# Kernel optimization log

Measured on AMD Instinct MI355X. Metric: run time of the kernel, lower is better.

The kernel has to match this reference:

```python
import jax, jax.numpy as jnp
import numpy as np

N = 100000      # num nodes
E = 1600000     # num edges (avg degree 16)
F_IN = 64       # n_input
F_H = 64        # n_hidden
K = 8           # Chebyshev order
LN_EPS = 1e-5


def setup_inputs() -> dict:
    key = jax.random.key(0)
    k1, k2, k3 = jax.random.split(key, 3)
    x = jax.random.normal(k1, (N, F_IN), dtype=jnp.float32)
    edge_index = jax.random.randint(k2, (2, E), 0, N, dtype=jnp.int32)
    # ChebConv learned params: K weight matrices + bias
    weight = jax.random.normal(k3, (K, F_IN, F_H), dtype=jnp.float32) * 0.05
    bias = jnp.zeros((F_H,), dtype=jnp.float32)
    # LayerNorm affine params
    ln_weight = jnp.ones((F_H,), dtype=jnp.float32)
    ln_bias = jnp.zeros((F_H,), dtype=jnp.float32)
    return {"x": x, "edge_index": edge_index, "weight": weight,
            "bias": bias, "ln_weight": ln_weight, "ln_bias": ln_bias}


def reference(x, edge_index, weight, bias, ln_weight, ln_bias):
    # ---- ChebConv with sym normalization, lambda_max = 2.0 (PyG default) ----
    # L_hat = 2L/lambda_max - I = (I - D^-1/2 A D^-1/2) - I = -D^-1/2 A D^-1/2
    # (self-loops removed before building the Laplacian, as in PyG)
    row, col = edge_index[0], edge_index[1]
    mask = (row != col)                                   # remove self loops
    ew = jnp.where(mask, 1.0, 0.0).astype(x.dtype)        # [E]
    deg = jax.ops.segment_sum(ew, row, num_segments=N)    # [N]
    dinv = jnp.where(deg > 0, jax.lax.rsqrt(jnp.maximum(deg, 1.0)), 0.0)
    w = -ew * dinv[row] * dinv[col]                       # L_hat edge weights [E]

    def prop(h):  # y = L_hat @ h  (sparse matvec via gather/scatter)
        return jax.ops.segment_sum(w[:, None] * h[col], row, num_segments=N)

    # Chebyshev recurrence: T0 = x, T1 = L_hat x, Tk = 2 L_hat T_{k-1} - T_{k-2}
    tx0 = x
    tx1 = prop(x)
    acc = tx0 @ weight[0] + tx1 @ weight[1]               # [N, F_H]

    def body(carry, Wk):
        tkm1, tkm2, acc = carry
        tk = 2.0 * prop(tkm1) - tkm2
        return (tk, tkm1, acc + tk @ Wk), None

    (_, _, acc), _ = jax.lax.scan(body, (tx1, tx0, acc), weight[2:])
    out = acc + bias

    # ---- LayerNorm(n_hidden) over feature dim ----
    mu = jnp.mean(out, axis=-1, keepdims=True)
    var = jnp.mean(jnp.square(out - mu), axis=-1, keepdims=True)
    h = (out - mu) * jax.lax.rsqrt(var + LN_EPS) * ln_weight + ln_bias

    # ---- ELU ----
    return jax.nn.elu(h)
```

## Files before the change

### kernel.cpp

```cpp
#include <hip/hip_runtime.h>
#include <math.h>

#define F 64
#define PR_ROWS 16

using short8 = __attribute__((ext_vector_type(8))) short;
using f32x4  = __attribute__((ext_vector_type(4))) float;

static __device__ __forceinline__ ushort f2bf(float f) {
    uint u = __float_as_uint(f);
    uint r = (u + 0x7fffu + ((u >> 16) & 1u)) >> 16;
    return (ushort)r;
}
static __device__ __forceinline__ float bf2f(ushort v) {
    return __uint_as_float(((uint)v) << 16);
}


__global__ __launch_bounds__(256) void deg_kernel(const int* __restrict__ ei, int E,
                                                  int* __restrict__ deg) {
    int e = blockIdx.x * 256 + threadIdx.x;
    if (e >= E) return;
    int r = ei[e], c = ei[E + e];
    if (r != c) atomicAdd(&deg[r], 1);
}

__global__ __launch_bounds__(256) void scan1_kernel(const int* __restrict__ deg,
                                                    int* __restrict__ rp,
                                                    int* __restrict__ bsum, int Nv) {
    __shared__ int sh[256];
    int t = threadIdx.x;
    int base = blockIdx.x * 1024 + t * 4;
    int v0 = (base + 0 < Nv) ? ((deg[base + 0] + 7) & ~7) : 0;
    int v1 = (base + 1 < Nv) ? ((deg[base + 1] + 7) & ~7) : 0;
    int v2 = (base + 2 < Nv) ? ((deg[base + 2] + 7) & ~7) : 0;
    int v3 = (base + 3 < Nv) ? ((deg[base + 3] + 7) & ~7) : 0;
    int s = v0 + v1 + v2 + v3;
    sh[t] = s;
    __syncthreads();
    for (int off = 1; off < 256; off <<= 1) {
        int a = (t >= off) ? sh[t - off] : 0;
        __syncthreads();
        sh[t] += a;
        __syncthreads();
    }
    int run = sh[t] - s;
    run += v0; if (base + 0 < Nv) rp[base + 1] = run;
    run += v1; if (base + 1 < Nv) rp[base + 2] = run;
    run += v2; if (base + 2 < Nv) rp[base + 3] = run;
    run += v3; if (base + 3 < Nv) rp[base + 4] = run;
    if (t == 255) bsum[blockIdx.x] = sh[255];
}

__global__ __launch_bounds__(256) void scan2_kernel(int* __restrict__ bsum, int nb) {
    __shared__ int sh[256];
    int t = threadIdx.x;
    int v = (t < nb) ? bsum[t] : 0;
    sh[t] = v;
    __syncthreads();
    for (int off = 1; off < 256; off <<= 1) {
        int a = (t >= off) ? sh[t - off] : 0;
        __syncthreads();
        sh[t] += a;
        __syncthreads();
    }
    if (t < nb) bsum[t] = sh[t] - v;
}

__global__ __launch_bounds__(256) void scan3_kernel(int* __restrict__ rp,
                                                    const int* __restrict__ bsum,
                                                    const int* __restrict__ deg,
                                                    float* __restrict__ dinv, int Nv) {
    int i = blockIdx.x * 256 + threadIdx.x;
    if (i == 0) rp[0] = 0;
    if (i < Nv) {
        rp[i + 1] += bsum[i >> 10];
        int d = deg[i];
        dinv[i] = d > 0 ? rsqrtf((float)d) : 0.f;
    }
}

__global__ __launch_bounds__(256) void scatter_kernel(const int* __restrict__ ei, int E,
                                                      const int* __restrict__ rp,
                                                      int* __restrict__ fill,
                                                      const float* __restrict__ dinv,
                                                      const int* __restrict__ deg,
                                                      int* __restrict__ ce, int Nv) {
    int e = blockIdx.x * 256 + threadIdx.x;
    if (e >= E) return;
    int r = ei[e], c = ei[E + e];
    if (r == c) return;
    int old = atomicAdd(&fill[r], 1);
    ce[rp[r] + old] = (dinv[c] > 0.f) ? c : Nv;
    if (old == deg[r] - 1) {
        int q = rp[r] + deg[r], qe = rp[r + 1];
        for (; q < qe; q++) ce[q] = Nv;
    }
}


__global__ __launch_bounds__(256) void tobf16_kernel(const float4* __restrict__ src,
                                                     ushort4* __restrict__ dst,
                                                     const float* __restrict__ dinv,
                                                     int n4, int Nv) {
    int i = blockIdx.x * 256 + threadIdx.x;
    if (i < 16) dst[(size_t)Nv * 16 + i] = make_ushort4(0, 0, 0, 0);
    if (i >= n4) return;
    int row = i >> 4;
    float dr = dinv[row];
    float sv = dr > 0.f ? dr : 1.f;
    float4 v = src[i];
    dst[i] = make_ushort4(f2bf(sv * v.x), f2bf(sv * v.y), f2bf(sv * v.z), f2bf(sv * v.w));
}


__global__ __launch_bounds__(256) void wconv_kernel(const float* __restrict__ W,
                                                    ushort* __restrict__ WbT, int KK) {
    int t = blockIdx.x * 256 + threadIdx.x;
    if (t >= KK * F) return;
    int col = t / KK, kk = t - col * KK;
    WbT[t] = f2bf(W[(size_t)kk * F + col]);
}


__global__ __launch_bounds__(256) void prop_v5(const ushort* __restrict__ Gsrc,
                                               const float* __restrict__ Tm2,
                                               float* __restrict__ Toutf,
                                               ushort* __restrict__ Gout,
                                               const int* __restrict__ rp,
                                               const int* __restrict__ ce,
                                               const float* __restrict__ dinv,
                                               int Nv, int first, int store_f) {
    __shared__ __align__(16) ushort ush[PR_ROWS][F];
    int wave = threadIdx.x >> 6, lane = threadIdx.x & 63;
    int rbase = blockIdx.x * PR_ROWS + wave * 4;

    if (blockIdx.x == 0 && threadIdx.x < 8)
        ((uint4*)(Gout + (size_t)Nv * F))[threadIdx.x] = make_uint4(0, 0, 0, 0);

    for (int r = 0; r < 4; r++) {
        int i = rbase + r;
        bool act = i < Nv;
        int ii = act ? i : 0;
        float dr = dinv[ii];
        float tm2 = first ? 0.f : Tm2[(size_t)ii * F + lane];
        int s = rp[ii], e = rp[ii + 1];
        float s0 = 0.f, s1 = 0.f, s2 = 0.f, s3 = 0.f;
        float s4 = 0.f, s5 = 0.f, s6 = 0.f, s7 = 0.f;
        for (int p = s; p < e; p += 8) {
            int4 q0 = *(const int4*)(ce + p);
            int4 q1 = *(const int4*)(ce + p + 4);
            s0 += bf2f(Gsrc[(size_t)q0.x * F + lane]);
            s1 += bf2f(Gsrc[(size_t)q0.y * F + lane]);
            s2 += bf2f(Gsrc[(size_t)q0.z * F + lane]);
            s3 += bf2f(Gsrc[(size_t)q0.w * F + lane]);
            s4 += bf2f(Gsrc[(size_t)q1.x * F + lane]);
            s5 += bf2f(Gsrc[(size_t)q1.y * F + lane]);
            s6 += bf2f(Gsrc[(size_t)q1.z * F + lane]);
            s7 += bf2f(Gsrc[(size_t)q1.w * F + lane]);
        }
        float sum = ((s0 + s1) + (s2 + s3)) + ((s4 + s5) + (s6 + s7));
        float raw = -dr * sum;
        float tk = first ? raw : fmaf(2.f, raw, -tm2);
        if (act && store_f) Toutf[(size_t)i * F + lane] = tk;
        float sv = dr > 0.f ? dr : 1.f;
        ush[wave * 4 + r][lane] = f2bf(sv * tk);
    }
    __syncthreads();
    int t = threadIdx.x;
    if (t < 128) {
        int row = t >> 3;
        if (blockIdx.x * PR_ROWS + row < Nv)
            ((uint4*)Gout)[(size_t)blockIdx.x * 128 + t] = ((const uint4*)ush)[t];
    }
}


template <int NSL, int FIRST, int LAST>
__global__ __launch_bounds__(256) void gemm_all(
    const ushort* __restrict__ g0, const ushort* __restrict__ g1,
    const ushort* __restrict__ g2, const ushort* __restrict__ g3,
    const ushort* __restrict__ g4, const ushort* __restrict__ g5,
    const ushort* __restrict__ g6, const ushort* __restrict__ g7,
    const ushort* __restrict__ WbT, int kkbase, int KK,
    float* __restrict__ out, const float* __restrict__ bias,
    const float* __restrict__ lnw, const float* __restrict__ lnb,
    const int* __restrict__ deg, int Nv) {
    const ushort* gs[8] = {g0, g1, g2, g3, g4, g5, g6, g7};
    int wave = threadIdx.x >> 6, lane = threadIdx.x & 63;
    int rbase = (blockIdx.x * 4 + wave) * 16;
    if (rbase >= Nv) return;
    int r15 = lane & 15, kg = lane >> 4;
    int arow = rbase + r15;
    if (arow >= Nv) arow = Nv - 1;

    f32x4 acc[4];
#pragma unroll
    for (int t = 0; t < 4; t++) acc[t] = (f32x4){0.f, 0.f, 0.f, 0.f};

#pragma unroll
    for (int st = 0; st < 2 * NSL; st++) {
        const ushort* A = gs[st >> 1];
        short8 a = *(const short8*)(A + (size_t)arow * F + (st & 1) * 32 + kg * 8);
#pragma unroll
        for (int t = 0; t < 4; t++) {
            int col = t * 16 + r15;
            short8 b = *(const short8*)(WbT + (size_t)col * KK + kkbase + st * 32 + kg * 8);
            acc[t] = __builtin_amdgcn_mfma_f32_16x16x32_bf16(a, b, acc[t], 0, 0, 0);
        }
    }

    if (!LAST) {
#pragma unroll
        for (int t = 0; t < 4; t++) {
            int col = t * 16 + r15;
#pragma unroll
            for (int j = 0; j < 4; j++) {
                int row = rbase + kg * 4 + j;
                if (row < Nv) {
                    size_t idx = (size_t)row * F + col;
                    out[idx] = FIRST ? acc[t][j] : out[idx] + acc[t][j];
                }
            }
        }
    } else {
        float bc[4], wc[4], gc[4];
#pragma unroll
        for (int t = 0; t < 4; t++) {
            int col = t * 16 + r15;
            bc[t] = bias[col]; wc[t] = lnw[col]; gc[t] = lnb[col];
        }
#pragma unroll
        for (int j = 0; j < 4; j++) {
            int row = rbase + kg * 4 + j;
            int rr = row < Nv ? row : Nv - 1;
            int dg = deg[rr];
            float sr = dg > 0 ? sqrtf((float)dg) : 1.f;
            float v[4];
            float s = 0.f;
#pragma unroll
            for (int t = 0; t < 4; t++) {
                int col = t * 16 + r15;
                float a_ = acc[t][j];
                if (!FIRST) a_ += out[(size_t)rr * F + col];
                v[t] = a_ * sr + bc[t];
                s += v[t];
            }
            s += __shfl_xor(s, 1, 64); s += __shfl_xor(s, 2, 64);
            s += __shfl_xor(s, 4, 64); s += __shfl_xor(s, 8, 64);
            float mu = s * (1.f / F);
            float q = 0.f;
#pragma unroll
            for (int t = 0; t < 4; t++) { float d = v[t] - mu; q += d * d; }
            q += __shfl_xor(q, 1, 64); q += __shfl_xor(q, 2, 64);
            q += __shfl_xor(q, 4, 64); q += __shfl_xor(q, 8, 64);
            float inv = rsqrtf(q * (1.f / F) + 1e-5f);
            if (row < Nv) {
#pragma unroll
                for (int t = 0; t < 4; t++) {
                    int col = t * 16 + r15;
                    float y = (v[t] - mu) * inv * wc[t] + gc[t];
                    out[(size_t)row * F + col] = y > 0.f ? y : expm1f(y);
                }
            }
        }
    }
}


extern "C" void kernel_launch(void* const* d_in, const int* in_sizes, int n_in,
                              void* d_out, int out_size, void* d_ws, size_t ws_size,
                              hipStream_t stream) {
    (void)n_in; (void)out_size;
    const float* x    = (const float*)d_in[0];
    const int*   ei   = (const int*)d_in[1];
    const float* W    = (const float*)d_in[2];
    const float* bias = (const float*)d_in[3];
    const float* lnw  = (const float*)d_in[4];
    const float* lnb  = (const float*)d_in[5];
    float* out = (float*)d_out;

    int Nv = in_sizes[0] / F;
    int E  = in_sizes[1] / 2;
    int K  = in_sizes[2] / (F * F);
    int KK = K * F;

    char* base = (char*)d_ws;
    size_t off = 0;
    auto alloc = [&](size_t b) -> void* {
        void* p = base + off;
        off += (b + 255) & ~(size_t)255;
        return p;
    };
    int*    degfill = (int*)alloc((size_t)2 * Nv * 4);
    int*    deg  = degfill;
    int*    fill = degfill + Nv;
    int*    rp   = (int*)alloc(((size_t)Nv + 1) * 4);
    int     nb   = (Nv + 1023) / 1024;
    int*    bsum = (int*)alloc((size_t)nb * 4);
    float*  dinv = (float*)alloc((size_t)Nv * 4);
    int*    ce   = (int*)alloc(((size_t)E + 8 * Nv) * 4);
    float*  Ta   = (float*)alloc((size_t)Nv * F * 4);
    float*  Tb   = (float*)alloc((size_t)Nv * F * 4);
    ushort* WbT  = (ushort*)alloc((size_t)KK * F * 2);
    size_t fixed = off;

    size_t gbytes = ((size_t)Nv + 1) * F * 2;
    size_t galign = (gbytes + 255) & ~(size_t)255;
    int full = (K == 8 && fixed + 8 * galign <= ws_size) ? 1 : 0;
    int nG = full ? 8 : 3;
    ushort* G[8];
    for (int i = 0; i < nG; i++) G[i] = (ushort*)alloc(gbytes);
    if (off > ws_size) return;

    hipMemsetAsync(degfill, 0, (size_t)2 * Nv * 4, stream);

    int gE = (E + 255) / 256, gN = (Nv + 255) / 256;
    deg_kernel<<<gE, 256, 0, stream>>>(ei, E, deg);
    scan1_kernel<<<nb, 256, 0, stream>>>(deg, rp, bsum, Nv);
    scan2_kernel<<<1, 256, 0, stream>>>(bsum, nb);
    scan3_kernel<<<gN, 256, 0, stream>>>(rp, bsum, deg, dinv, Nv);
    scatter_kernel<<<gE, 256, 0, stream>>>(ei, E, rp, fill, dinv, deg, ce, Nv);

    int n4 = (Nv * F) / 4;
    tobf16_kernel<<<(n4 + 255) / 256, 256, 0, stream>>>((const float4*)x, (ushort4*)G[0],
                                                        dinv, n4, Nv);
    wconv_kernel<<<(KK * F + 255) / 256, 256, 0, stream>>>(W, WbT, KK);

    int gP = (Nv + PR_ROWS - 1) / PR_ROWS;
    int gG = (Nv + 63) / 64;

    for (int k = 1; k < K; k++) {
        float* tof = (k & 1) ? Ta : Tb;
        const float* tm2 = (k < 2) ? nullptr : (k == 2 ? x : (const float*)tof);
        int store_f = (k <= K - 3) ? 1 : 0;
        const ushort* gsrc = full ? G[k - 1] : G[(k - 1) % 3];
        ushort*       gdst = full ? G[k]     : G[k % 3];
        prop_v5<<<gP, 256, 0, stream>>>(gsrc, tm2, tof, gdst, rp, ce, dinv,
                                        Nv, k == 1 ? 1 : 0, store_f);
        if (!full && (k & 1)) {
            int p = k >> 1;
            const ushort* a0 = G[(2 * p) % 3];
            const ushort* a1 = G[(2 * p + 1) % 3];
            if (p == 0)
                gemm_all<2, 1, 0><<<gG, 256, 0, stream>>>(a0, a1, 0, 0, 0, 0, 0, 0,
                    WbT, p * 128, KK, out, bias, lnw, lnb, deg, Nv);
            else if (k < K - 1)
                gemm_all<2, 0, 0><<<gG, 256, 0, stream>>>(a0, a1, 0, 0, 0, 0, 0, 0,
                    WbT, p * 128, KK, out, bias, lnw, lnb, deg, Nv);
            else
                gemm_all<2, 0, 1><<<gG, 256, 0, stream>>>(a0, a1, 0, 0, 0, 0, 0, 0,
                    WbT, p * 128, KK, out, bias, lnw, lnb, deg, Nv);
        }
    }
    if (full)
        gemm_all<8, 1, 1><<<gG, 256, 0, stream>>>(G[0], G[1], G[2], G[3],
                                                  G[4], G[5], G[6], G[7],
                                                  WbT, 0, KK, out, bias, lnw, lnb,
                                                  deg, Nv);
}
```

Measured before the change: 551.3 us.

## Drop fp32 Chebyshev state; rebuild T_{k-2} from scaled bf16 buffers and fuse init

```diff
diff --git a/kernel.cpp b/kernel.cpp
--- a/kernel.cpp
+++ b/kernel.cpp
@@ -99,38 +99,39 @@
 }
 
 
-__global__ __launch_bounds__(256) void tobf16_kernel(const float4* __restrict__ src,
-                                                     ushort4* __restrict__ dst,
-                                                     const float* __restrict__ dinv,
-                                                     int n4, int Nv) {
+__global__ __launch_bounds__(256) void init_kernel(const float4* __restrict__ src,
+                                                   ushort4* __restrict__ dst,
+                                                   const float* __restrict__ dinv,
+                                                   const float* __restrict__ W,
+                                                   ushort* __restrict__ WbT,
+                                                   int n4, int KK, int Nv) {
     int i = blockIdx.x * 256 + threadIdx.x;
     if (i < 16) dst[(size_t)Nv * 16 + i] = make_ushort4(0, 0, 0, 0);
-    if (i >= n4) return;
-    int row = i >> 4;
-    float dr = dinv[row];
-    float sv = dr > 0.f ? dr : 1.f;
-    float4 v = src[i];
-    dst[i] = make_ushort4(f2bf(sv * v.x), f2bf(sv * v.y), f2bf(sv * v.z), f2bf(sv * v.w));
-}
-
-
-__global__ __launch_bounds__(256) void wconv_kernel(const float* __restrict__ W,
-                                                    ushort* __restrict__ WbT, int KK) {
-    int t = blockIdx.x * 256 + threadIdx.x;
-    if (t >= KK * F) return;
-    int col = t / KK, kk = t - col * KK;
-    WbT[t] = f2bf(W[(size_t)kk * F + col]);
-}
-
-
-__global__ __launch_bounds__(256) void prop_v5(const ushort* __restrict__ Gsrc,
-                                               const float* __restrict__ Tm2,
-                                               float* __restrict__ Toutf,
+    if (i < n4) {
+        int row = i >> 4;
+        float dr = dinv[row];
+        float sv = dr > 0.f ? dr : 1.f;
+        float4 v = src[i];
+        dst[i] = make_ushort4(f2bf(sv * v.x), f2bf(sv * v.y),
+                              f2bf(sv * v.z), f2bf(sv * v.w));
+        return;
+    }
+    int t = i - n4;
+    if (t < KK * F) {
+        int col = t / KK, kk = t - col * KK;
+        WbT[t] = f2bf(W[(size_t)kk * F + col]);
+    }
+}
+
+
+__global__ __launch_bounds__(256) void prop_v7(const ushort* __restrict__ Gsrc,
+                                               const ushort* __restrict__ Gm2,
                                                ushort* __restrict__ Gout,
                                                const int* __restrict__ rp,
                                                const int* __restrict__ ce,
                                                const float* __restrict__ dinv,
-                                               int Nv, int first, int store_f) {
+                                               const int* __restrict__ deg,
+                                               int Nv, int first) {
     __shared__ __align__(16) ushort ush[PR_ROWS][F];
     int wave = threadIdx.x >> 6, lane = threadIdx.x & 63;
     int rbase = blockIdx.x * PR_ROWS + wave * 4;
@@ -143,7 +144,9 @@
         bool act = i < Nv;
         int ii = act ? i : 0;
         float dr = dinv[ii];
-        float tm2 = first ? 0.f : Tm2[(size_t)ii * F + lane];
+        int dg = deg[ii];
+        float sr = dg > 0 ? sqrtf((float)dg) : 1.f;
+        float tm2 = first ? 0.f : sr * bf2f(Gm2[(size_t)ii * F + lane]);
         int s = rp[ii], e = rp[ii + 1];
         float s0 = 0.f, s1 = 0.f, s2 = 0.f, s3 = 0.f;
         float s4 = 0.f, s5 = 0.f, s6 = 0.f, s7 = 0.f;
@@ -162,7 +165,6 @@
         float sum = ((s0 + s1) + (s2 + s3)) + ((s4 + s5) + (s6 + s7));
         float raw = -dr * sum;
         float tk = first ? raw : fmaf(2.f, raw, -tm2);
-        if (act && store_f) Toutf[(size_t)i * F + lane] = tk;
         float sv = dr > 0.f ? dr : 1.f;
         ush[wave * 4 + r][lane] = f2bf(sv * tk);
     }
@@ -300,8 +302,6 @@
     int*    bsum = (int*)alloc((size_t)nb * 4);
     float*  dinv = (float*)alloc((size_t)Nv * 4);
     int*    ce   = (int*)alloc(((size_t)E + 8 * Nv) * 4);
-    float*  Ta   = (float*)alloc((size_t)Nv * F * 4);
-    float*  Tb   = (float*)alloc((size_t)Nv * F * 4);
     ushort* WbT  = (ushort*)alloc((size_t)KK * F * 2);
     size_t fixed = off;
 
@@ -323,21 +323,20 @@
     scatter_kernel<<<gE, 256, 0, stream>>>(ei, E, rp, fill, dinv, deg, ce, Nv);
 
     int n4 = (Nv * F) / 4;
-    tobf16_kernel<<<(n4 + 255) / 256, 256, 0, stream>>>((const float4*)x, (ushort4*)G[0],
-                                                        dinv, n4, Nv);
-    wconv_kernel<<<(KK * F + 255) / 256, 256, 0, stream>>>(W, WbT, KK);
+    int initN = n4 + KK * F;
+    init_kernel<<<(initN + 255) / 256, 256, 0, stream>>>((const float4*)x, (ushort4*)G[0],
+                                                         dinv, W, WbT, n4, KK, Nv);
 
     int gP = (Nv + PR_ROWS - 1) / PR_ROWS;
     int gG = (Nv + 63) / 64;
 
     for (int k = 1; k < K; k++) {
-        float* tof = (k & 1) ? Ta : Tb;
-        const float* tm2 = (k < 2) ? nullptr : (k == 2 ? x : (const float*)tof);
-        int store_f = (k <= K - 3) ? 1 : 0;
         const ushort* gsrc = full ? G[k - 1] : G[(k - 1) % 3];
-        ushort*       gdst = full ? G[k]     : G[k % 3];
-        prop_v5<<<gP, 256, 0, stream>>>(gsrc, tm2, tof, gdst, rp, ce, dinv,
-                                        Nv, k == 1 ? 1 : 0, store_f);
+        const ushort* gm2  = (k < 2) ? (const ushort*)nullptr
+                                     : (full ? G[k - 2] : G[(k - 2) % 3]);
+        ushort*       gdst = full ? G[k] : G[k % 3];
+        prop_v7<<<gP, 256, 0, stream>>>(gsrc, gm2, gdst, rp, ce, dinv, deg,
+                                        Nv, k == 1 ? 1 : 0);
         if (!full && (k & 1)) {
             int p = k >> 1;
             const ushort* a0 = G[(2 * p) % 3];
```

Result: no change. 561.4 us (+1.8%).
